# Performance work log

Measured on AMD Instinct MI355X. Metric: run time of the kernel, lower is better.

The kernel has to match this reference:

```python
import jax, jax.numpy as jnp
import numpy as np

B, L, D, H = 8, 1024, 1024, 16
K = D // H

def setup_inputs() -> dict:
    key = jax.random.key(0)
    k1, k2, k3 = jax.random.split(key, 3)
    scale = 1.0 / np.sqrt(D)
    return {
        "x": jax.random.normal(k1, (B, L, D), dtype=jnp.float32),
        "w_in": jax.random.normal(k2, (D, 3 * D), dtype=jnp.float32) * scale,
        "b_in": jnp.zeros((3 * D,), dtype=jnp.float32),
        "w_out": jax.random.normal(k3, (D, D), dtype=jnp.float32) * scale,
        "b_out": jnp.zeros((D,), dtype=jnp.float32),
    }

def reference(x, w_in, b_in, w_out, b_out):
    # Fused QKV projection: [B, L, 3D]
    qkv = x @ w_in + b_in
    q, k, v = jnp.split(qkv, 3, axis=-1)
    # [B, L, D] -> [B, H, L, K]
    def to_heads(t):
        return t.reshape(B, L, H, K).transpose(0, 2, 1, 3)
    q, k, v = to_heads(q), to_heads(k), to_heads(v)
    # Full [B, H, L, L] score matrix (non-flash, as in source)
    logits = jnp.einsum('bhlk,bhmk->bhlm', q, k) / jnp.sqrt(jnp.float32(K))
    # NOTE: the source computes softmax but then (bug, reproduced faithfully)
    # uses the raw logits in the value contraction. causal_mask defaults False.
    out = jnp.einsum('bhlm,bhmk->bhlk', logits, v)
    out = out.transpose(0, 2, 1, 3).reshape(B, L, D)
    return out @ w_out + b_out
```

## Files before the change

### kernel.cpp

```cpp
#include <hip/hip_runtime.h>
#include <hip/hip_bf16.h>


typedef __attribute__((ext_vector_type(8))) short short8;
typedef __attribute__((ext_vector_type(4))) float f32x4;

static __device__ __forceinline__ short f2bf(float f) {
  __hip_bfloat16 h = __float2bfloat16(f);
  return __builtin_bit_cast(short, h);
}
static __device__ __forceinline__ float bf2f(short s) {
  unsigned int u = ((unsigned int)(unsigned short)s) << 16;
  return __builtin_bit_cast(float, u);
}

static __device__ __forceinline__ void gload_lds16(const void* g, void* l) {
  __builtin_amdgcn_global_load_lds(
      (const __attribute__((address_space(1))) void*)g,
      (__attribute__((address_space(3))) void*)l, 16, 0, 0);
}

__global__ __launch_bounds__(256) void cast_f32_bf16_kernel(
    const float* __restrict__ in, __hip_bfloat16* __restrict__ out) {
  size_t i = ((size_t)blockIdx.x * 256 + threadIdx.x) * 8;
  float4 v0 = *(const float4*)(in + i);
  float4 v1 = *(const float4*)(in + i + 4);
  short8 o;
  o[0] = f2bf(v0.x); o[1] = f2bf(v0.y); o[2] = f2bf(v0.z); o[3] = f2bf(v0.w);
  o[4] = f2bf(v1.x); o[5] = f2bf(v1.y); o[6] = f2bf(v1.z); o[7] = f2bf(v1.w);
  *(short8*)((__hip_bfloat16*)out + i) = o;
}

__global__ __launch_bounds__(256) void transpose_cast_kernel(
    const float* __restrict__ in, __hip_bfloat16* __restrict__ out, int R, int C) {
  __shared__ float tile[32][33];
  int c0 = blockIdx.x * 32, r0 = blockIdx.y * 32;
  int tx = threadIdx.x & 31;
  int ty = threadIdx.x >> 5;
#pragma unroll
  for (int i = 0; i < 4; ++i)
    tile[ty + i * 8][tx] = in[(size_t)(r0 + ty + i * 8) * C + c0 + tx];
  __syncthreads();
#pragma unroll
  for (int i = 0; i < 4; ++i)
    out[(size_t)(c0 + ty + i * 8) * R + r0 + tx] =
        __float2bfloat16(tile[tx][ty + i * 8]);
}

static __device__ __forceinline__ void store_out(__hip_bfloat16* p, float v) {
  *p = __float2bfloat16(v);
}
static __device__ __forceinline__ void store_out(float* p, float v) { *p = v; }

template <typename OutT>
__global__ __launch_bounds__(256) void gemm_bt_kernel(
    const __hip_bfloat16* __restrict__ A, const __hip_bfloat16* __restrict__ Bt,
    const float* __restrict__ bias, OutT* __restrict__ C,
    int M, int N, int Kd) {
  __shared__ __align__(16) __hip_bfloat16 As[128 * 32];
  __shared__ __align__(16) __hip_bfloat16 Bs[128 * 32];

  const int t = threadIdx.x;
  const int bn = blockIdx.x, bm = blockIdx.y;
  const int m0 = bm * 128, n0 = bn * 128;
  const int w = t >> 6, lane = t & 63;
  const int wr = w >> 1, wc = w & 1;
  const int lr = lane & 15, kg = lane >> 4;

  const int g0 = w * 128 + lane;
  const int g1 = g0 + 64;
  const int rowA0 = g0 >> 2, kgp0 = g0 & 3;
  const int rowA1 = g1 >> 2, kgp1 = g1 & 3;
  __hip_bfloat16* ldsA0 = As + (size_t)(w * 128) * 8;
  __hip_bfloat16* ldsA1 = As + (size_t)(w * 128 + 64) * 8;
  __hip_bfloat16* ldsB0 = Bs + (size_t)(w * 128) * 8;
  __hip_bfloat16* ldsB1 = Bs + (size_t)(w * 128 + 64) * 8;

  f32x4 acc[4][4] = {};

  const int steps = Kd >> 5;
  for (int kt = 0; kt < steps; ++kt) {
    const int kcolb = kt * 32;
    gload_lds16(A + (size_t)(m0 + rowA0) * Kd + kcolb + kgp0 * 8, ldsA0);
    gload_lds16(A + (size_t)(m0 + rowA1) * Kd + kcolb + kgp1 * 8, ldsA1);
    gload_lds16(Bt + (size_t)(n0 + rowA0) * Kd + kcolb + kgp0 * 8, ldsB0);
    gload_lds16(Bt + (size_t)(n0 + rowA1) * Kd + kcolb + kgp1 * 8, ldsB1);
    __syncthreads();

    short8 af[4], bfv[4];
#pragma unroll
    for (int mi = 0; mi < 4; ++mi)
      af[mi] = *(const short8*)&As[(wr * 64 + mi * 16 + lr) * 32 + kg * 8];
#pragma unroll
    for (int ni = 0; ni < 4; ++ni)
      bfv[ni] = *(const short8*)&Bs[(wc * 64 + ni * 16 + lr) * 32 + kg * 8];
#pragma unroll
    for (int mi = 0; mi < 4; ++mi)
#pragma unroll
      for (int ni = 0; ni < 4; ++ni)
        acc[mi][ni] = __builtin_amdgcn_mfma_f32_16x16x32_bf16(
            af[mi], bfv[ni], acc[mi][ni], 0, 0, 0);
    __syncthreads();
  }

#pragma unroll
  for (int mi = 0; mi < 4; ++mi) {
    int row0 = m0 + wr * 64 + mi * 16 + kg * 4;
#pragma unroll
    for (int ni = 0; ni < 4; ++ni) {
      int col = n0 + wc * 64 + ni * 16 + lr;
      float bv = bias[col];
#pragma unroll
      for (int r = 0; r < 4; ++r)
        store_out(&C[(size_t)(row0 + r) * N + col], acc[mi][ni][r] + bv);
    }
  }
}

__global__ __launch_bounds__(256) void ktv_kernel(
    const __hip_bfloat16* __restrict__ qkv, float* __restrict__ Spart) {
  __shared__ __align__(16) float Ks[64][68];
  __shared__ __align__(16) float Vs[64][68];
  const int bh = blockIdx.x;
  const int ch = blockIdx.y;
  const int b = bh >> 4, h = bh & 15;
  const __hip_bfloat16* base = qkv + (size_t)b * 1024 * 3072;
  const int hoff = h * 64;
  const int t = threadIdx.x;
  const int i0 = (t >> 4) * 4;
  const int j0 = (t & 15) * 4;
  const int srow = t >> 2;
  const int sg0 = t & 3;

  f32x4 acc[4] = {};

  for (int c = 0; c < 2; ++c) {
    int l0 = ch * 128 + c * 64;
#pragma unroll
    for (int rep = 0; rep < 2; ++rep) {
      int g = sg0 + rep * 4;
      const __hip_bfloat16* rowp = base + (size_t)(l0 + srow) * 3072;
      short8 kv = *(const short8*)(rowp + 1024 + hoff + g * 8);
      short8 vv = *(const short8*)(rowp + 2048 + hoff + g * 8);
      f32x4 k0, k1, v0, v1;
#pragma unroll
      for (int e = 0; e < 4; ++e) {
        k0[e] = bf2f(kv[e]); k1[e] = bf2f(kv[4 + e]);
        v0[e] = bf2f(vv[e]); v1[e] = bf2f(vv[4 + e]);
      }
      *(f32x4*)&Ks[srow][g * 8] = k0;
      *(f32x4*)&Ks[srow][g * 8 + 4] = k1;
      *(f32x4*)&Vs[srow][g * 8] = v0;
      *(f32x4*)&Vs[srow][g * 8 + 4] = v1;
    }
    __syncthreads();
#pragma unroll 8
    for (int l = 0; l < 64; ++l) {
      f32x4 kq = *(const f32x4*)&Ks[l][i0];
      f32x4 vq = *(const f32x4*)&Vs[l][j0];
#pragma unroll
      for (int ii = 0; ii < 4; ++ii) acc[ii] += kq[ii] * vq;
    }
    __syncthreads();
  }

  float* Sp = Spart + ((size_t)ch * 128 + bh) * 4096;
#pragma unroll
  for (int ii = 0; ii < 4; ++ii)
#pragma unroll
    for (int jj = 0; jj < 4; ++jj)
      Sp[(i0 + ii) * 64 + j0 + jj] = acc[ii][jj];
}

__global__ __launch_bounds__(256) void qs_kernel(
    const __hip_bfloat16* __restrict__ qkv, const float* __restrict__ Spart,
    __hip_bfloat16* __restrict__ attn) {
  __shared__ __align__(16) float Ql[128][68];
  __shared__ __align__(16) float Sl[64][68];
  const int bh = blockIdx.x;
  const int rblk = blockIdx.y;
  const int b = bh >> 4, h = bh & 15;
  const __hip_bfloat16* Qp = qkv + (size_t)b * 1024 * 3072 + h * 64;
  const int r0 = rblk * 128;
  const int t = threadIdx.x;

#pragma unroll
  for (int rep = 0; rep < 4; ++rep) {
    int g = t + rep * 256;
    int row = g >> 3, gg = g & 7;
    short8 qv = *(const short8*)(Qp + (size_t)(r0 + row) * 3072 + gg * 8);
    f32x4 f0, f1;
#pragma unroll
    for (int e = 0; e < 4; ++e) { f0[e] = bf2f(qv[e]); f1[e] = bf2f(qv[4 + e]); }
    *(f32x4*)&Ql[row][gg * 8] = f0;
    *(f32x4*)&Ql[row][gg * 8 + 4] = f1;
  }
#pragma unroll
  for (int rep = 0; rep < 4; ++rep) {
    int g = t + rep * 256;
    int row = g >> 4, gg = g & 15;
    f32x4 s = {};
#pragma unroll
    for (int c = 0; c < 8; ++c)
      s += *(const f32x4*)&Spart[((size_t)c * 128 + bh) * 4096 + row * 64 + gg * 4];
    *(f32x4*)&Sl[row][gg * 4] = s * 0.125f;
  }
  __syncthreads();

  const int rt0 = (t >> 3) * 4;
  const int j0 = (t & 7) * 8;
  f32x4 accA[4] = {}, accB[4] = {};
#pragma unroll 4
  for (int i = 0; i < 64; i += 4) {
    f32x4 q[4], s0[4], s1[4];
#pragma unroll
    for (int rr = 0; rr < 4; ++rr) q[rr] = *(const f32x4*)&Ql[rt0 + rr][i];
#pragma unroll
    for (int ii = 0; ii < 4; ++ii) {
      s0[ii] = *(const f32x4*)&Sl[i + ii][j0];
      s1[ii] = *(const f32x4*)&Sl[i + ii][j0 + 4];
    }
#pragma unroll
    for (int ii = 0; ii < 4; ++ii)
#pragma unroll
      for (int rr = 0; rr < 4; ++rr) {
        accA[rr] += q[rr][ii] * s0[ii];
        accB[rr] += q[rr][ii] * s1[ii];
      }
  }

#pragma unroll
  for (int rr = 0; rr < 4; ++rr) {
    short8 o;
#pragma unroll
    for (int e = 0; e < 4; ++e) {
      o[e] = f2bf(accA[rr][e]);
      o[4 + e] = f2bf(accB[rr][e]);
    }
    *(short8*)(attn + (size_t)(b * 1024 + r0 + rt0 + rr) * 1024 + h * 64 + j0) = o;
  }
}

extern "C" void kernel_launch(void* const* d_in, const int* in_sizes, int n_in,
                              void* d_out, int out_size, void* d_ws, size_t ws_size,
                              hipStream_t stream) {
  const float* x = (const float*)d_in[0];
  const float* w_in = (const float*)d_in[1];
  const float* b_in = (const float*)d_in[2];
  const float* w_out = (const float*)d_in[3];
  const float* b_out = (const float*)d_in[4];
  float* out = (float*)d_out;

  char* ws = (char*)d_ws;
  __hip_bfloat16* x_bf = (__hip_bfloat16*)ws;   ws += (size_t)8192 * 1024 * 2;
  __hip_bfloat16* w_inT = (__hip_bfloat16*)ws;  ws += (size_t)3072 * 1024 * 2;
  __hip_bfloat16* w_outT = (__hip_bfloat16*)ws; ws += (size_t)1024 * 1024 * 2;
  __hip_bfloat16* qkv = (__hip_bfloat16*)ws;    ws += (size_t)8192 * 3072 * 2;
  float* Spart = (float*)ws;                    ws += (size_t)8 * 128 * 64 * 64 * 4;
  __hip_bfloat16* attn = (__hip_bfloat16*)ws;   ws += (size_t)8192 * 1024 * 2;

  cast_f32_bf16_kernel<<<4096, 256, 0, stream>>>(x, x_bf);
  transpose_cast_kernel<<<dim3(96, 32), 256, 0, stream>>>(w_in, w_inT, 1024, 3072);
  transpose_cast_kernel<<<dim3(32, 32), 256, 0, stream>>>(w_out, w_outT, 1024, 1024);

  gemm_bt_kernel<__hip_bfloat16><<<dim3(24, 64), 256, 0, stream>>>(
      x_bf, w_inT, b_in, qkv, 8192, 3072, 1024);

  ktv_kernel<<<dim3(128, 8), 256, 0, stream>>>(qkv, Spart);

  qs_kernel<<<dim3(128, 8), 256, 0, stream>>>(qkv, Spart, attn);

  gemm_bt_kernel<float><<<dim3(8, 64), 256, 0, stream>>>(
      attn, w_outT, b_out, out, 8192, 1024, 1024);
}
```

Baseline: 162.0 us.

## Replace GEMM with 256x256-tile, 8-wave, double-buffered pipelined kernel

Swaps the simple 128x128 single-buffered GEMM for a 256x256-tile, 512-thread kernel. It double-buffers A/B in LDS and interleaves direct-to-LDS global loads with MFMA phases, using explicit barriers, waitcnt and sched_barrier. Workgroup IDs are remapped so neighbouring blocks land on the same XCD, and setprio is raised around the MFMA bursts. The aim is to hide global load latency and reuse more data per tile in both projection GEMMs. The price is heavier register and LDS pressure, fewer workgroups (384 and 128), and a fragile hand-written schedule; the output GEMM with 128 blocks may underfill the chip.

```diff
diff --git a/kernel.cpp b/kernel.cpp
--- a/kernel.cpp
+++ b/kernel.cpp
@@ -14,11 +14,14 @@
   return __builtin_bit_cast(float, u);
 }
 
-static __device__ __forceinline__ void gload_lds16(const void* g, void* l) {
-  __builtin_amdgcn_global_load_lds(
-      (const __attribute__((address_space(1))) void*)g,
-      (__attribute__((address_space(3))) void*)l, 16, 0, 0);
-}
+#define GLOAD16(src, dst)                                        \
+  __builtin_amdgcn_global_load_lds(                              \
+      (const __attribute__((address_space(1))) void*)(src),      \
+      (__attribute__((address_space(3))) void*)(dst), 16, 0, 0)
+#define BAR() __builtin_amdgcn_s_barrier()
+#define SCHED() __builtin_amdgcn_sched_barrier(0)
+#define WAIT_LGKM0() asm volatile("s_waitcnt lgkmcnt(0)" ::: "memory")
+#define WAIT_VM6() asm volatile("s_waitcnt vmcnt(6)" ::: "memory")
 
 __global__ __launch_bounds__(256) void cast_f32_bf16_kernel(
     const float* __restrict__ in, __hip_bfloat16* __restrict__ out) {
@@ -53,66 +56,141 @@
 static __device__ __forceinline__ void store_out(float* p, float v) { *p = v; }
 
 template <typename OutT>
-__global__ __launch_bounds__(256) void gemm_bt_kernel(
+__global__ __launch_bounds__(512, 2) void gemm8p_kernel(
     const __hip_bfloat16* __restrict__ A, const __hip_bfloat16* __restrict__ Bt,
     const float* __restrict__ bias, OutT* __restrict__ C,
-    int M, int N, int Kd) {
-  __shared__ __align__(16) __hip_bfloat16 As[128 * 32];
-  __shared__ __align__(16) __hip_bfloat16 Bs[128 * 32];
+    int M, int N, int Kd, int ntn) {
+  __shared__ short8 sA[2][2048];
+  __shared__ short8 sB[2][2048];
 
   const int t = threadIdx.x;
-  const int bn = blockIdx.x, bm = blockIdx.y;
-  const int m0 = bm * 128, n0 = bn * 128;
   const int w = t >> 6, lane = t & 63;
-  const int wr = w >> 1, wc = w & 1;
+  const int wm = w >> 2, wn = w & 3;
+
+  const int nwg = gridDim.x, cpx = nwg >> 3;
+  const int wg = (blockIdx.x & 7) * cpx + (blockIdx.x >> 3);
+  const int bm = wg / ntn, bn = wg % ntn;
+  const size_t m0 = (size_t)bm * 256, n0 = (size_t)bn * 256;
+
+  int srow[2], skc[2];
+#pragma unroll
+  for (int i = 0; i < 2; ++i) {
+    int g = i * 512 + t;
+    int st = g >> 6;
+    srow[i] = (st >> 1) * 16 + ((g >> 2) & 15);
+    skc[i] = (st & 1) * 32 + (g & 3) * 8;
+  }
+  const int perm = (lane & 15) * 4 + (lane >> 4);
+
+  const int kTiles = Kd >> 6;
+  const int kMask = kTiles - 1;
+
+  f32x4 acc[8][4] = {};
+  short8 aF[4][2], bF[4][2];
+
+  auto stageA = [&](int buf, int h, int kt) {
+#pragma unroll
+    for (int i = 0; i < 2; ++i)
+      GLOAD16(A + (m0 + h * 128 + srow[i]) * (size_t)Kd + kt * 64 + skc[i],
+              &sA[buf][h * 1024 + i * 512 + w * 64]);
+  };
+  auto stageB = [&](int buf, int h, int kt) {
+#pragma unroll
+    for (int i = 0; i < 2; ++i)
+      GLOAD16(Bt + (n0 + h * 128 + srow[i]) * (size_t)Kd + kt * 64 + skc[i],
+              &sB[buf][h * 1024 + i * 512 + w * 64]);
+  };
+  auto readA = [&](int buf, int miBase) {
+#pragma unroll
+    for (int mi = 0; mi < 4; ++mi)
+#pragma unroll
+      for (int kk = 0; kk < 2; ++kk)
+        aF[mi][kk] = sA[buf][wm * 1024 + ((miBase + mi) * 2 + kk) * 64 + perm];
+  };
+  auto readB = [&](int buf) {
+#pragma unroll
+    for (int ni = 0; ni < 4; ++ni)
+#pragma unroll
+      for (int kk = 0; kk < 2; ++kk)
+        bF[ni][kk] =
+            sB[buf][(wn >> 1) * 1024 + (((wn & 1) * 4 + ni) * 2 + kk) * 64 + perm];
+  };
+  auto mfma16 = [&](int miBase, int niBase) {
+    __builtin_amdgcn_s_setprio(1);
+#pragma unroll
+    for (int kk = 0; kk < 2; ++kk)
+#pragma unroll
+      for (int ni = 0; ni < 2; ++ni)
+#pragma unroll
+        for (int mi = 0; mi < 4; ++mi)
+          acc[miBase + mi][niBase + ni] = __builtin_amdgcn_mfma_f32_16x16x32_bf16(
+              aF[mi][kk], bF[niBase + ni][kk], acc[miBase + mi][niBase + ni],
+              0, 0, 0);
+    __builtin_amdgcn_s_setprio(0);
+  };
+
+  stageA(0, 0, 0); stageA(0, 1, 0); stageB(0, 0, 0); stageB(0, 1, 0);
+  stageB(1, 0, 1); stageB(1, 1, 1); stageA(1, 0, 1);
+  WAIT_VM6();
+  SCHED();
+  BAR();
+  SCHED();
+
+  for (int it = 0; it < kTiles / 2; ++it) {
+    const int t1 = 2 * it + 1;
+    const int t2 = (2 * it + 2) & kMask;
+    const int t3 = (2 * it + 3) & kMask;
+    readB(0); readA(0, 0);
+    stageA(1, 1, t1);
+    BAR(); SCHED(); WAIT_LGKM0(); SCHED();
+    mfma16(0, 0);
+    BAR(); SCHED();
+    stageB(0, 0, t2);
+    BAR(); SCHED();
+    mfma16(0, 2);
+    BAR(); SCHED();
+    readA(0, 4);
+    stageB(0, 1, t2);
+    BAR(); SCHED(); WAIT_LGKM0(); SCHED();
+    mfma16(4, 0);
+    BAR(); SCHED();
+    stageA(0, 0, t2);
+    WAIT_VM6(); SCHED();
+    BAR(); SCHED();
+    mfma16(4, 2);
+    BAR(); SCHED();
+    readB(1); readA(1, 0);
+    stageA(0, 1, t2);
+    BAR(); SCHED(); WAIT_LGKM0(); SCHED();
+    mfma16(0, 0);
+    BAR(); SCHED();
+    stageB(1, 0, t3);
+    BAR(); SCHED();
+    mfma16(0, 2);
+    BAR(); SCHED();
+    readA(1, 4);
+    stageB(1, 1, t3);
+    BAR(); SCHED(); WAIT_LGKM0(); SCHED();
+    mfma16(4, 0);
+    BAR(); SCHED();
+    stageA(1, 0, t3);
+    WAIT_VM6(); SCHED();
+    BAR(); SCHED();
+    mfma16(4, 2);
+    BAR(); SCHED();
+  }
+
   const int lr = lane & 15, kg = lane >> 4;
-
-  const int g0 = w * 128 + lane;
-  const int g1 = g0 + 64;
-  const int rowA0 = g0 >> 2, kgp0 = g0 & 3;
-  const int rowA1 = g1 >> 2, kgp1 = g1 & 3;
-  __hip_bfloat16* ldsA0 = As + (size_t)(w * 128) * 8;
-  __hip_bfloat16* ldsA1 = As + (size_t)(w * 128 + 64) * 8;
-  __hip_bfloat16* ldsB0 = Bs + (size_t)(w * 128) * 8;
-  __hip_bfloat16* ldsB1 = Bs + (size_t)(w * 128 + 64) * 8;
-
-  f32x4 acc[4][4] = {};
-
-  const int steps = Kd >> 5;
-  for (int kt = 0; kt < steps; ++kt) {
-    const int kcolb = kt * 32;
-    gload_lds16(A + (size_t)(m0 + rowA0) * Kd + kcolb + kgp0 * 8, ldsA0);
-    gload_lds16(A + (size_t)(m0 + rowA1) * Kd + kcolb + kgp1 * 8, ldsA1);
-    gload_lds16(Bt + (size_t)(n0 + rowA0) * Kd + kcolb + kgp0 * 8, ldsB0);
-    gload_lds16(Bt + (size_t)(n0 + rowA1) * Kd + kcolb + kgp1 * 8, ldsB1);
-    __syncthreads();
-
-    short8 af[4], bfv[4];
-#pragma unroll
-    for (int mi = 0; mi < 4; ++mi)
-      af[mi] = *(const short8*)&As[(wr * 64 + mi * 16 + lr) * 32 + kg * 8];
-#pragma unroll
-    for (int ni = 0; ni < 4; ++ni)
-      bfv[ni] = *(const short8*)&Bs[(wc * 64 + ni * 16 + lr) * 32 + kg * 8];
-#pragma unroll
-    for (int mi = 0; mi < 4; ++mi)
-#pragma unroll
-      for (int ni = 0; ni < 4; ++ni)
-        acc[mi][ni] = __builtin_amdgcn_mfma_f32_16x16x32_bf16(
-            af[mi], bfv[ni], acc[mi][ni], 0, 0, 0);
-    __syncthreads();
-  }
-
-#pragma unroll
-  for (int mi = 0; mi < 4; ++mi) {
-    int row0 = m0 + wr * 64 + mi * 16 + kg * 4;
+#pragma unroll
+  for (int mi = 0; mi < 8; ++mi) {
+    size_t row0 = m0 + wm * 128 + mi * 16 + kg * 4;
 #pragma unroll
     for (int ni = 0; ni < 4; ++ni) {
-      int col = n0 + wc * 64 + ni * 16 + lr;
+      size_t col = n0 + wn * 64 + ni * 16 + lr;
       float bv = bias[col];
 #pragma unroll
       for (int r = 0; r < 4; ++r)
-        store_out(&C[(size_t)(row0 + r) * N + col], acc[mi][ni][r] + bv);
+        store_out(&C[(row0 + r) * N + col], acc[mi][ni][r] + bv);
     }
   }
 }
@@ -263,13 +341,12 @@
   transpose_cast_kernel<<<dim3(96, 32), 256, 0, stream>>>(w_in, w_inT, 1024, 3072);
   transpose_cast_kernel<<<dim3(32, 32), 256, 0, stream>>>(w_out, w_outT, 1024, 1024);
 
-  gemm_bt_kernel<__hip_bfloat16><<<dim3(24, 64), 256, 0, stream>>>(
-      x_bf, w_inT, b_in, qkv, 8192, 3072, 1024);
+  gemm8p_kernel<__hip_bfloat16><<<32 * 12, 512, 0, stream>>>(
+      x_bf, w_inT, b_in, qkv, 8192, 3072, 1024, 12);
 
   ktv_kernel<<<dim3(128, 8), 256, 0, stream>>>(qkv, Spart);
-
   qs_kernel<<<dim3(128, 8), 256, 0, stream>>>(qkv, Spart, attn);
 
-  gemm_bt_kernel<float><<<dim3(8, 64), 256, 0, stream>>>(
-      attn, w_outT, b_out, out, 8192, 1024, 1024);
-}
+  gemm8p_kernel<float><<<32 * 4, 512, 0, stream>>>(
+      attn, w_outT, b_out, out, 8192, 1024, 1024, 4);
+}
```

Result: slower. 170.8 us (+5.4%).

## Fold per-head KtV state into output projection weights, skip attn intermediate

Applied to the files above, without the earlier changes.

Instead of computing Q·S per head into an attn buffer and then projecting with w_out, a new kernel premultiplies each batch's per-head S (K^T V) into w_out to form a per-batch projection matrix Ut. The final GEMM then reads Q directly from the qkv buffer with a batched Bt. This removes the qs kernel and the attn round trip in exchange for a per-batch 1024x1024 weight matrix. The GEMM also gains compile-time shapes, incremental source pointers, and an XCD-aware block swizzle across the 8 XCDs. S is rounded to bf16 before the fold, which adds a small precision loss.

```diff
diff --git a/kernel.cpp b/kernel.cpp
--- a/kernel.cpp
+++ b/kernel.cpp
@@ -14,11 +14,10 @@
   return __builtin_bit_cast(float, u);
 }
 
-static __device__ __forceinline__ void gload_lds16(const void* g, void* l) {
-  __builtin_amdgcn_global_load_lds(
-      (const __attribute__((address_space(1))) void*)g,
-      (__attribute__((address_space(3))) void*)l, 16, 0, 0);
-}
+#define GLOAD16(src, dst)                                        \
+  __builtin_amdgcn_global_load_lds(                              \
+      (const __attribute__((address_space(1))) void*)(src),      \
+      (__attribute__((address_space(3))) void*)(dst), 16, 0, 0)
 
 __global__ __launch_bounds__(256) void cast_f32_bf16_kernel(
     const float* __restrict__ in, __hip_bfloat16* __restrict__ out) {
@@ -52,25 +51,33 @@
 }
 static __device__ __forceinline__ void store_out(float* p, float v) { *p = v; }
 
-template <typename OutT>
+template <typename OutT, int KD, int AS, int NBN, int NOUT, long BTB>
 __global__ __launch_bounds__(256) void gemm_bt_kernel(
     const __hip_bfloat16* __restrict__ A, const __hip_bfloat16* __restrict__ Bt,
-    const float* __restrict__ bias, OutT* __restrict__ C,
-    int M, int N, int Kd) {
+    const float* __restrict__ bias, OutT* __restrict__ C) {
   __shared__ __align__(16) __hip_bfloat16 As[128 * 32];
   __shared__ __align__(16) __hip_bfloat16 Bs[128 * 32];
 
   const int t = threadIdx.x;
-  const int bn = blockIdx.x, bm = blockIdx.y;
+  A += (size_t)blockIdx.y * 1024 * AS;
+  Bt += (size_t)blockIdx.y * BTB;
+  C += (size_t)blockIdx.y * 1024 * NOUT;
+
+  const int cpx = gridDim.x >> 3;
+  const int wg = (blockIdx.x & 7) * cpx + (blockIdx.x >> 3);
+  const int bm = wg / NBN, bn = wg % NBN;
   const int m0 = bm * 128, n0 = bn * 128;
+
   const int w = t >> 6, lane = t & 63;
   const int wr = w >> 1, wc = w & 1;
   const int lr = lane & 15, kg = lane >> 4;
 
   const int g0 = w * 128 + lane;
   const int g1 = g0 + 64;
-  const int rowA0 = g0 >> 2, kgp0 = g0 & 3;
-  const int rowA1 = g1 >> 2, kgp1 = g1 & 3;
+  const __hip_bfloat16* srcA0 = A + (size_t)(m0 + (g0 >> 2)) * AS + (g0 & 3) * 8;
+  const __hip_bfloat16* srcA1 = A + (size_t)(m0 + (g1 >> 2)) * AS + (g1 & 3) * 8;
+  const __hip_bfloat16* srcB0 = Bt + (size_t)(n0 + (g0 >> 2)) * KD + (g0 & 3) * 8;
+  const __hip_bfloat16* srcB1 = Bt + (size_t)(n0 + (g1 >> 2)) * KD + (g1 & 3) * 8;
   __hip_bfloat16* ldsA0 = As + (size_t)(w * 128) * 8;
   __hip_bfloat16* ldsA1 = As + (size_t)(w * 128 + 64) * 8;
   __hip_bfloat16* ldsB0 = Bs + (size_t)(w * 128) * 8;
@@ -78,13 +85,13 @@
 
   f32x4 acc[4][4] = {};
 
-  const int steps = Kd >> 5;
-  for (int kt = 0; kt < steps; ++kt) {
-    const int kcolb = kt * 32;
-    gload_lds16(A + (size_t)(m0 + rowA0) * Kd + kcolb + kgp0 * 8, ldsA0);
-    gload_lds16(A + (size_t)(m0 + rowA1) * Kd + kcolb + kgp1 * 8, ldsA1);
-    gload_lds16(Bt + (size_t)(n0 + rowA0) * Kd + kcolb + kgp0 * 8, ldsB0);
-    gload_lds16(Bt + (size_t)(n0 + rowA1) * Kd + kcolb + kgp1 * 8, ldsB1);
+#pragma unroll 1
+  for (int kt = 0; kt < KD / 32; ++kt) {
+    GLOAD16(srcA0, ldsA0);
+    GLOAD16(srcA1, ldsA1);
+    GLOAD16(srcB0, ldsB0);
+    GLOAD16(srcB1, ldsB1);
+    srcA0 += 32; srcA1 += 32; srcB0 += 32; srcB1 += 32;
     __syncthreads();
 
     short8 af[4], bfv[4];
@@ -112,7 +119,7 @@
       float bv = bias[col];
 #pragma unroll
       for (int r = 0; r < 4; ++r)
-        store_out(&C[(size_t)(row0 + r) * N + col], acc[mi][ni][r] + bv);
+        store_out(&C[(size_t)(row0 + r) * NOUT + col], acc[mi][ni][r] + bv);
     }
   }
 }
@@ -172,72 +179,62 @@
       Sp[(i0 + ii) * 64 + j0 + jj] = acc[ii][jj];
 }
 
-__global__ __launch_bounds__(256) void qs_kernel(
-    const __hip_bfloat16* __restrict__ qkv, const float* __restrict__ Spart,
-    __hip_bfloat16* __restrict__ attn) {
-  __shared__ __align__(16) float Ql[128][68];
-  __shared__ __align__(16) float Sl[64][68];
+__global__ __launch_bounds__(512) void ut_kernel(
+    const float* __restrict__ Spart, const __hip_bfloat16* __restrict__ w_outT,
+    __hip_bfloat16* __restrict__ Ut) {
+  __shared__ __align__(16) __hip_bfloat16 Sl[64][72];
   const int bh = blockIdx.x;
-  const int rblk = blockIdx.y;
   const int b = bh >> 4, h = bh & 15;
-  const __hip_bfloat16* Qp = qkv + (size_t)b * 1024 * 3072 + h * 64;
-  const int r0 = rblk * 128;
-  const int t = threadIdx.x;
-
-#pragma unroll
-  for (int rep = 0; rep < 4; ++rep) {
-    int g = t + rep * 256;
-    int row = g >> 3, gg = g & 7;
-    short8 qv = *(const short8*)(Qp + (size_t)(r0 + row) * 3072 + gg * 8);
-    f32x4 f0, f1;
-#pragma unroll
-    for (int e = 0; e < 4; ++e) { f0[e] = bf2f(qv[e]); f1[e] = bf2f(qv[4 + e]); }
-    *(f32x4*)&Ql[row][gg * 8] = f0;
-    *(f32x4*)&Ql[row][gg * 8 + 4] = f1;
-  }
-#pragma unroll
-  for (int rep = 0; rep < 4; ++rep) {
-    int g = t + rep * 256;
-    int row = g >> 4, gg = g & 15;
+  const int t = threadIdx.x, w = t >> 6, lane = t & 63;
+  const int lr = lane & 15, kg = lane >> 4;
+
+#pragma unroll
+  for (int rep = 0; rep < 2; ++rep) {
+    int e4 = t + rep * 512;
+    int row = e4 >> 4, c4 = e4 & 15;
     f32x4 s = {};
 #pragma unroll
     for (int c = 0; c < 8; ++c)
-      s += *(const f32x4*)&Spart[((size_t)c * 128 + bh) * 4096 + row * 64 + gg * 4];
-    *(f32x4*)&Sl[row][gg * 4] = s * 0.125f;
+      s += *(const f32x4*)&Spart[((size_t)c * 128 + bh) * 4096 + row * 64 + c4 * 4];
+    s *= 0.125f;
+    __hip_bfloat16* p = &Sl[row][c4 * 4];
+    p[0] = __float2bfloat16(s[0]); p[1] = __float2bfloat16(s[1]);
+    p[2] = __float2bfloat16(s[2]); p[3] = __float2bfloat16(s[3]);
   }
   __syncthreads();
 
-  const int rt0 = (t >> 3) * 4;
-  const int j0 = (t & 7) * 8;
-  f32x4 accA[4] = {}, accB[4] = {};
-#pragma unroll 4
-  for (int i = 0; i < 64; i += 4) {
-    f32x4 q[4], s0[4], s1[4];
-#pragma unroll
-    for (int rr = 0; rr < 4; ++rr) q[rr] = *(const f32x4*)&Ql[rt0 + rr][i];
-#pragma unroll
-    for (int ii = 0; ii < 4; ++ii) {
-      s0[ii] = *(const f32x4*)&Sl[i + ii][j0];
-      s1[ii] = *(const f32x4*)&Sl[i + ii][j0 + 4];
-    }
-#pragma unroll
-    for (int ii = 0; ii < 4; ++ii)
-#pragma unroll
-      for (int rr = 0; rr < 4; ++rr) {
-        accA[rr] += q[rr][ii] * s0[ii];
-        accB[rr] += q[rr][ii] * s1[ii];
-      }
-  }
-
-#pragma unroll
-  for (int rr = 0; rr < 4; ++rr) {
-    short8 o;
-#pragma unroll
-    for (int e = 0; e < 4; ++e) {
-      o[e] = f2bf(accA[rr][e]);
-      o[4 + e] = f2bf(accB[rr][e]);
-    }
-    *(short8*)(attn + (size_t)(b * 1024 + r0 + rt0 + rr) * 1024 + h * 64 + j0) = o;
+  const __hip_bfloat16* Ap = w_outT + (size_t)(w * 128 + lr) * 1024 + h * 64 + kg * 8;
+  short8 bF[4][2];
+#pragma unroll
+  for (int ni = 0; ni < 4; ++ni)
+#pragma unroll
+    for (int kk = 0; kk < 2; ++kk)
+      bF[ni][kk] = *(const short8*)&Sl[ni * 16 + lr][kk * 32 + kg * 8];
+
+  f32x4 acc[8][4] = {};
+#pragma unroll
+  for (int mi = 0; mi < 8; ++mi) {
+#pragma unroll
+    for (int kk = 0; kk < 2; ++kk) {
+      short8 aF = *(const short8*)(Ap + (size_t)mi * 16 * 1024 + kk * 32);
+#pragma unroll
+      for (int ni = 0; ni < 4; ++ni)
+        acc[mi][ni] = __builtin_amdgcn_mfma_f32_16x16x32_bf16(
+            aF, bF[ni][kk], acc[mi][ni], 0, 0, 0);
+    }
+  }
+
+  __hip_bfloat16* Up = Ut + (size_t)b * 1024 * 1024;
+#pragma unroll
+  for (int mi = 0; mi < 8; ++mi) {
+    int row0 = w * 128 + mi * 16 + kg * 4;
+#pragma unroll
+    for (int ni = 0; ni < 4; ++ni) {
+      int col = h * 64 + ni * 16 + lr;
+#pragma unroll
+      for (int r = 0; r < 4; ++r)
+        Up[(size_t)(row0 + r) * 1024 + col] = __float2bfloat16(acc[mi][ni][r]);
+    }
   }
 }
 
@@ -257,19 +254,19 @@
   __hip_bfloat16* w_outT = (__hip_bfloat16*)ws; ws += (size_t)1024 * 1024 * 2;
   __hip_bfloat16* qkv = (__hip_bfloat16*)ws;    ws += (size_t)8192 * 3072 * 2;
   float* Spart = (float*)ws;                    ws += (size_t)8 * 128 * 64 * 64 * 4;
-  __hip_bfloat16* attn = (__hip_bfloat16*)ws;   ws += (size_t)8192 * 1024 * 2;
+  __hip_bfloat16* Ut = (__hip_bfloat16*)ws;     ws += (size_t)8 * 1024 * 1024 * 2;
 
   cast_f32_bf16_kernel<<<4096, 256, 0, stream>>>(x, x_bf);
   transpose_cast_kernel<<<dim3(96, 32), 256, 0, stream>>>(w_in, w_inT, 1024, 3072);
   transpose_cast_kernel<<<dim3(32, 32), 256, 0, stream>>>(w_out, w_outT, 1024, 1024);
 
-  gemm_bt_kernel<__hip_bfloat16><<<dim3(24, 64), 256, 0, stream>>>(
-      x_bf, w_inT, b_in, qkv, 8192, 3072, 1024);
+  gemm_bt_kernel<__hip_bfloat16, 1024, 1024, 24, 3072, 0>
+      <<<dim3(1536, 1), 256, 0, stream>>>(x_bf, w_inT, b_in, qkv);
 
   ktv_kernel<<<dim3(128, 8), 256, 0, stream>>>(qkv, Spart);
 
-  qs_kernel<<<dim3(128, 8), 256, 0, stream>>>(qkv, Spart, attn);
-
-  gemm_bt_kernel<float><<<dim3(8, 64), 256, 0, stream>>>(
-      attn, w_outT, b_out, out, 8192, 1024, 1024);
-}
+  ut_kernel<<<128, 512, 0, stream>>>(Spart, w_outT, Ut);
+
+  gemm_bt_kernel<float, 1024, 3072, 8, 1024, 1024 * 1024>
+      <<<dim3(64, 8), 256, 0, stream>>>(qkv, Ut, b_out, out);
+}
```

After: 156.0 us. 1.04x faster.
